# Kernel tuning notes

Measured on AMD Instinct MI355X. Metric: run time of the kernel, lower is better.

## Reference

```python
import jax, jax.numpy as jnp
import numpy as np

DECAY = 0.1  # P['decay']


def setup_inputs() -> dict:
    key = jax.random.key(0)
    k0, k1, k2, k3, k4 = jax.random.split(key, 5)
    N, B, T = 512, 64, 1024
    hidden_0 = jax.random.normal(k0, (N,), dtype=jnp.float32)
    Batch_Input = jax.random.normal(k1, (B, T, N), dtype=jnp.float32)
    # scale recurrent weight ~1/sqrt(N) so the leaky-tanh dynamics stay bounded
    W = jax.random.normal(k2, (N, N), dtype=jnp.float32) / np.sqrt(N).astype(np.float32)
    Gw = jax.random.normal(k3, (2, N), dtype=jnp.float32)
    Gb = jax.random.normal(k4, (2,), dtype=jnp.float32)
    return {"hidden_0": hidden_0, "Batch_Input": Batch_Input, "W": W, "Gw": Gw, "Gb": Gb}


def reference(hidden_0, Batch_Input, W, Gw, Gb):
    B, T, N = Batch_Input.shape
    h0 = jnp.broadcast_to(hidden_0[None, :], (B, N))  # repeat over batch
    xs = jnp.swapaxes(Batch_Input, 0, 1)  # [T, B, N] for scan over time

    def step(h, x):
        # h_new = (1-d)*h + d*(tanh(h) @ W^T + x)   (einsum 'ab,cb->ca')
        h_new = (1.0 - DECAY) * h + DECAY * (jnp.tanh(h) @ W.T + x)
        return h_new, jnp.tanh(h_new)

    _, hidden_t = jax.lax.scan(step, h0, xs)  # hidden_t: [T, B, N]
    geometry = hidden_t @ Gw.T + Gb  # [T, B, 2]
    return jnp.swapaxes(hidden_t, 0, 1), jnp.swapaxes(geometry, 0, 1)
```

## Files before the change

### kernel.cpp

```cpp
#include <hip/hip_runtime.h>
#include <hip/hip_fp16.h>
#include <cmath>

#define RN 512
#define RT 1024
#define RB 64
#define SMEM_BYTES 86016

typedef _Float16 half2v __attribute__((ext_vector_type(2)));

__device__ __forceinline__ float fast_tanh(float x) {
    float e = __expf(2.0f * x);
    return 1.0f - 2.0f / (e + 1.0f);
}
__device__ __forceinline__ unsigned pack2(float a, float b) {
    return (unsigned)__half_as_ushort(__float2half(a)) |
           ((unsigned)__half_as_ushort(__float2half(b)) << 16);
}
__device__ __forceinline__ unsigned pkrtz(float a, float b) {
    auto h = __builtin_amdgcn_cvt_pkrtz(a, b);
    return __builtin_bit_cast(unsigned, h);
}
__device__ __forceinline__ float dot2(unsigned wa, unsigned tb, float acc) {
    half2v a = __builtin_bit_cast(half2v, wa);
    half2v b = __builtin_bit_cast(half2v, tb);
    return __builtin_amdgcn_fdot2(a, b, acc, false);
}
template <int CTRL>
__device__ __forceinline__ float dpp_add(float x) {
    int p = __builtin_amdgcn_update_dpp(0, __float_as_int(x), CTRL, 0xf, 0xf, true);
    return x + __int_as_float(p);
}
__device__ __forceinline__ float red16(float x) {
    x = dpp_add<0xB1>(x);
    x = dpp_add<0x4E>(x);
    x = dpp_add<0x141>(x);
    x = dpp_add<0x140>(x);
    return x;
}
#define D2Q(acc, wq, tq) \
    acc = dot2((wq).x, (tq).x, acc); acc = dot2((wq).y, (tq).y, acc); \
    acc = dot2((wq).z, (tq).z, acc); acc = dot2((wq).w, (tq).w, acc);

#define PIN4(v) asm volatile("" : "+v"((v).x), "+v"((v).y), "+v"((v).z), "+v"((v).w));

#define LOADB(bb) { \
    const int b_ = (part + (bb)) & 3; \
    w##bb##_0 = wsrc[(b_ * 4 + 0) * 512]; PIN4(w##bb##_0) \
    w##bb##_1 = wsrc[(b_ * 4 + 1) * 512]; PIN4(w##bb##_1) \
    w##bb##_2 = wsrc[(b_ * 4 + 2) * 512]; PIN4(w##bb##_2) \
    w##bb##_3 = wsrc[(b_ * 4 + 3) * 512]; PIN4(w##bb##_3) }

#define DOTB(bb, tv) \
    D2Q(acc0, w##bb##_0, tv) D2Q(acc1, w##bb##_1, tv) \
    D2Q(acc2, w##bb##_2, tv) D2Q(acc3, w##bb##_3, tv)

__global__ void __launch_bounds__(512, 1) rnn_step_kernel(
    const float* __restrict__ h0,
    const float* __restrict__ X,
    const uint4* __restrict__ Wpk,
    const float* __restrict__ tanh0,
    float* __restrict__ outH,
    unsigned* __restrict__ ctr,
    unsigned* __restrict__ xcdctr)
{
    extern __shared__ unsigned char smem[];
    unsigned* ownpk = (unsigned*)smem;
    int*      bc    = (int*)(smem + 256);
    unsigned* lctr  = (unsigned*)(smem + 264);

    const int tid = threadIdx.x;
    if (tid == 0) {
        unsigned xcd;
        asm volatile("s_getreg_b32 %0, hwreg(HW_REG_XCC_ID)" : "=s"(xcd));
        xcd &= 7u;
        unsigned rank = __hip_atomic_fetch_add(&xcdctr[xcd], 1u,
                            __ATOMIC_RELAXED, __HIP_MEMORY_SCOPE_AGENT) & 31u;
        int slot = (int)(xcd * 32u + rank);
        bc[0] = slot >> 2;
        bc[1] = slot & 3;
        *lctr = 0u;
    }
    __syncthreads();
    const int batch = bc[0], part = bc[1];

    uint4 w0_0, w0_1, w0_2, w0_3;
    uint4 w1_0, w1_1, w1_2, w1_3;
    uint4 w2_0, w2_1, w2_2, w2_3;
    uint4 w3_0, w3_1, w3_2, w3_3;
    {
        const uint4* wsrc = Wpk + part * 8192 + tid;
        LOADB(0) LOADB(1) LOADB(2) LOADB(3)
    }

    const int rg = tid >> 4;
    const int kc = tid & 15;
    const int row0 = part * 128 + rg * 4;

    const float* srcB  = tanh0;
    const float* xPtr  = X    + (size_t)batch * RT * RN + row0;
    float*       oPtr  = outH + (size_t)batch * RT * RN + row0;
    const float* oBase = outH + (size_t)batch * RT * RN;

    float4 h = {0, 0, 0, 0};
    float4 xv = {0, 0, 0, 0};
    if (kc == 0) {
        h = *reinterpret_cast<const float4*>(h0 + row0);
        float t0 = tanhf(h.x), t1 = tanhf(h.y), t2 = tanhf(h.z), t3 = tanhf(h.w);
        ownpk[2 * rg]     = pack2(t0, t1);
        ownpk[2 * rg + 1] = pack2(t2, t3);
        xv = *reinterpret_cast<const float4*>(xPtr);
    }

    unsigned* gctr = ctr + batch * 32;
    __syncthreads();

    #pragma unroll 1
    for (int t = 0; t < RT; ++t) {
        float4 xn = {0, 0, 0, 0};
        if (kc == 0) {
            const float* xnp = (t + 1 < RT) ? (xPtr + RN) : xPtr;
            xn = *reinterpret_cast<const float4*>(xnp);
        }

        float acc0 = 0.f, acc1 = 0.f, acc2 = 0.f, acc3 = 0.f;
        {
            uint4 th = *reinterpret_cast<const uint4*>(&ownpk[4 * kc]);
            DOTB(0, th)
        }

        if (tid == 0 && t > 0) {
            const unsigned tgt = 4u * (unsigned)t;
            while (__hip_atomic_load(gctr, __ATOMIC_RELAXED,
                                     __HIP_MEMORY_SCOPE_AGENT) < tgt)
                __builtin_amdgcn_s_sleep(1);
        }
        __syncthreads();

        {
            const int b1 = (part + 1) & 3;
            const float* p = srcB + b1 * 128 + kc * 8;
            float4 f0 = *reinterpret_cast<const float4*>(p);
            float4 f1 = *reinterpret_cast<const float4*>(p + 4);
            uint4 tv = make_uint4(pkrtz(f0.x, f0.y), pkrtz(f0.z, f0.w),
                                  pkrtz(f1.x, f1.y), pkrtz(f1.z, f1.w));
            DOTB(1, tv)
        }
        {
            const int b2 = (part + 2) & 3;
            const float* p = srcB + b2 * 128 + kc * 8;
            float4 f0 = *reinterpret_cast<const float4*>(p);
            float4 f1 = *reinterpret_cast<const float4*>(p + 4);
            uint4 tv = make_uint4(pkrtz(f0.x, f0.y), pkrtz(f0.z, f0.w),
                                  pkrtz(f1.x, f1.y), pkrtz(f1.z, f1.w));
            DOTB(2, tv)
        }
        {
            const int b3 = (part + 3) & 3;
            const float* p = srcB + b3 * 128 + kc * 8;
            float4 f0 = *reinterpret_cast<const float4*>(p);
            float4 f1 = *reinterpret_cast<const float4*>(p + 4);
            uint4 tv = make_uint4(pkrtz(f0.x, f0.y), pkrtz(f0.z, f0.w),
                                  pkrtz(f1.x, f1.y), pkrtz(f1.z, f1.w));
            DOTB(3, tv)
        }

        acc0 = red16(acc0); acc1 = red16(acc1);
        acc2 = red16(acc2); acc3 = red16(acc3);

        if (kc == 0) {
            h.x = 0.9f * h.x + 0.1f * (acc0 + xv.x);
            h.y = 0.9f * h.y + 0.1f * (acc1 + xv.y);
            h.z = 0.9f * h.z + 0.1f * (acc2 + xv.z);
            h.w = 0.9f * h.w + 0.1f * (acc3 + xv.w);
            float t0 = fast_tanh(h.x), t1 = fast_tanh(h.y);
            float t2 = fast_tanh(h.z), t3 = fast_tanh(h.w);
            *reinterpret_cast<float4*>(oPtr) = make_float4(t0, t1, t2, t3);
            ownpk[2 * rg]     = pack2(t0, t1);
            ownpk[2 * rg + 1] = pack2(t2, t3);
        }

        asm volatile("s_waitcnt vmcnt(0)" ::: "memory");
        if ((tid & 63) == 0) {
            unsigned a = __hip_atomic_fetch_add(lctr, 1u, __ATOMIC_RELAXED,
                                                __HIP_MEMORY_SCOPE_WORKGROUP);
            if ((a & 7u) == 7u)
                __hip_atomic_fetch_add(gctr, 1u, __ATOMIC_RELAXED,
                                       __HIP_MEMORY_SCOPE_AGENT);
        }
        __syncthreads();
        xv = xn;

        srcB = (t == 0) ? oBase : (srcB + RN);
        xPtr += RN;
        oPtr += RN;
    }
}

__global__ void pack_w(const float* __restrict__ W, uint4* __restrict__ Wpk)
{
    int o = blockIdx.x * blockDim.x + threadIdx.x;
    if (o >= 32768) return;
    int part = o >> 13;
    int b    = (o >> 11) & 3;
    int i    = (o >> 9) & 3;
    int tid  = o & 511;
    int row  = part * 128 + (tid >> 4) * 4 + i;
    int k0   = b * 128 + (tid & 15) * 8;
    const float* s = W + (size_t)row * RN + k0;
    uint4 v;
    v.x = pack2(s[0], s[1]); v.y = pack2(s[2], s[3]);
    v.z = pack2(s[4], s[5]); v.w = pack2(s[6], s[7]);
    Wpk[o] = v;
}

__global__ void geom_kernel(const float* __restrict__ hid,
                            const float* __restrict__ Gw,
                            const float* __restrict__ Gb,
                            float* __restrict__ geo)
{
    const int wid  = (blockIdx.x * blockDim.x + threadIdx.x) >> 6;
    const int lane = threadIdx.x & 63;
    if (wid >= RB * RT) return;
    const float* rowp = hid + (size_t)wid * RN;
    float g0 = 0.f, g1 = 0.f;
    #pragma unroll
    for (int j = 0; j < 8; ++j) {
        float v = rowp[lane + 64 * j];
        g0 = fmaf(v, Gw[lane + 64 * j], g0);
        g1 = fmaf(v, Gw[RN + lane + 64 * j], g1);
    }
    #pragma unroll
    for (int m = 32; m >= 1; m >>= 1) {
        g0 += __shfl_xor(g0, m);
        g1 += __shfl_xor(g1, m);
    }
    if (lane == 0) {
        geo[(size_t)wid * 2]     = g0 + Gb[0];
        geo[(size_t)wid * 2 + 1] = g1 + Gb[1];
    }
}

__global__ void init_misc(const float* __restrict__ h0,
                          float* __restrict__ tanh0,
                          unsigned* __restrict__ ctr,
                          unsigned* __restrict__ xcdctr)
{
    int i = blockIdx.x * blockDim.x + threadIdx.x;
    if (i < RN) tanh0[i] = tanhf(h0[i]);
    if (i < RB * 32) ctr[i] = 0u;
    if (i < 8) xcdctr[i] = 0u;
}

extern "C" void kernel_launch(void* const* d_in, const int* in_sizes, int n_in,
                              void* d_out, int out_size, void* d_ws, size_t ws_size,
                              hipStream_t stream)
{
    const float* h0 = (const float*)d_in[0];
    const float* X  = (const float*)d_in[1];
    const float* W  = (const float*)d_in[2];
    const float* Gw = (const float*)d_in[3];
    const float* Gb = (const float*)d_in[4];

    float* outH = (float*)d_out;
    float* geo  = outH + (size_t)RB * RT * RN;

    float*    tanh0  = (float*)d_ws;
    unsigned* ctr    = (unsigned*)d_ws + RN;
    unsigned* xcdctr = ctr + RB * 32;
    uint4*    Wpk    = (uint4*)(((uintptr_t)(xcdctr + 8) + 63) & ~(uintptr_t)63);

    (void)hipFuncSetAttribute((const void*)rnn_step_kernel,
                              hipFuncAttributeMaxDynamicSharedMemorySize, SMEM_BYTES);

    pack_w<<<64, 512, 0, stream>>>(W, Wpk);
    init_misc<<<8, 512, 0, stream>>>(h0, tanh0, ctr, xcdctr);

    void* kargs[] = { (void*)&h0, (void*)&X, (void*)&Wpk, (void*)&tanh0,
                      (void*)&outH, (void*)&ctr, (void*)&xcdctr };
    (void)hipLaunchCooperativeKernel(rnn_step_kernel, dim3(256), dim3(512),
                                     kargs, SMEM_BYTES, stream);

    geom_kernel<<<(RB * RT * 64 + 255) / 256, 256, 0, stream>>>(outH, Gw, Gb, geo);
}
```

Baseline: 1.859 ms.

## Split each batch's recurrence across two workgroups instead of four

Each batch sequence is now handled by 2 workgroups of 256 rows each, rather than 4 workgroups of 128 rows. Each thread keeps twice as many packed fp16 weights in registers and computes 8 output rows. The upper half of the launched blocks exit immediately, and the cross-workgroup spin barrier now waits for 2 arrivals per step with no sleep. This halves the per-step cross-block synchronisation and global reads of peers' tanh outputs, but doubles per-step compute and register pressure per workgroup and leaves only 128 active CUs.

```diff
diff --git a/kernel.cpp b/kernel.cpp
--- a/kernel.cpp
+++ b/kernel.cpp
@@ -44,16 +44,20 @@
 
 #define PIN4(v) asm volatile("" : "+v"((v).x), "+v"((v).y), "+v"((v).z), "+v"((v).w));
 
-#define LOADB(bb) { \
-    const int b_ = (part + (bb)) & 3; \
-    w##bb##_0 = wsrc[(b_ * 4 + 0) * 512]; PIN4(w##bb##_0) \
-    w##bb##_1 = wsrc[(b_ * 4 + 1) * 512]; PIN4(w##bb##_1) \
-    w##bb##_2 = wsrc[(b_ * 4 + 2) * 512]; PIN4(w##bb##_2) \
-    w##bb##_3 = wsrc[(b_ * 4 + 3) * 512]; PIN4(w##bb##_3) }
-
-#define DOTB(bb, tv) \
-    D2Q(acc0, w##bb##_0, tv) D2Q(acc1, w##bb##_1, tv) \
-    D2Q(acc2, w##bb##_2, tv) D2Q(acc3, w##bb##_3, tv)
+#define DECLW(pre) uint4 pre##0_0, pre##0_1, pre##1_0, pre##1_1, pre##2_0, pre##2_1, \
+    pre##3_0, pre##3_1, pre##4_0, pre##4_1, pre##5_0, pre##5_1, pre##6_0, pre##6_1, \
+    pre##7_0, pre##7_1;
+
+#define LW(pre, base, r) \
+    pre##r##_0 = (base)[((r)*2 + 0) * 512]; PIN4(pre##r##_0) \
+    pre##r##_1 = (base)[((r)*2 + 1) * 512]; PIN4(pre##r##_1)
+
+#define LOADALL(pre, base) \
+    LW(pre, base, 0) LW(pre, base, 1) LW(pre, base, 2) LW(pre, base, 3) \
+    LW(pre, base, 4) LW(pre, base, 5) LW(pre, base, 6) LW(pre, base, 7)
+
+#define DOTA(r) D2Q(a##r, wa##r##_0, th0) D2Q(a##r, wa##r##_1, th1)
+#define DOTBq(r) D2Q(a##r, wb##r##_0, tb0) D2Q(a##r, wb##r##_1, tb1)
 
 __global__ void __launch_bounds__(512, 1) rnn_step_kernel(
     const float* __restrict__ h0,
@@ -66,8 +70,8 @@
 {
     extern __shared__ unsigned char smem[];
     unsigned* ownpk = (unsigned*)smem;
-    int*      bc    = (int*)(smem + 256);
-    unsigned* lctr  = (unsigned*)(smem + 264);
+    int*      bc    = (int*)(smem + 512);
+    unsigned* lctr  = (unsigned*)(smem + 528);
 
     const int tid = threadIdx.x;
     if (tid == 0) {
@@ -76,40 +80,49 @@
         xcd &= 7u;
         unsigned rank = __hip_atomic_fetch_add(&xcdctr[xcd], 1u,
                             __ATOMIC_RELAXED, __HIP_MEMORY_SCOPE_AGENT) & 31u;
-        int slot = (int)(xcd * 32u + rank);
-        bc[0] = slot >> 2;
-        bc[1] = slot & 3;
+        if (rank < 16u) {
+            int slot = (int)(xcd * 16u + rank);
+            bc[0] = slot >> 1;
+            bc[1] = slot & 1;
+            bc[2] = 1;
+        } else {
+            bc[2] = 0;
+        }
         *lctr = 0u;
     }
     __syncthreads();
+    if (bc[2] == 0) return;
     const int batch = bc[0], part = bc[1];
-
-    uint4 w0_0, w0_1, w0_2, w0_3;
-    uint4 w1_0, w1_1, w1_2, w1_3;
-    uint4 w2_0, w2_1, w2_2, w2_3;
-    uint4 w3_0, w3_1, w3_2, w3_3;
+    const int hfp = 1 - part;
+
+    DECLW(wa) DECLW(wb)
     {
-        const uint4* wsrc = Wpk + part * 8192 + tid;
-        LOADB(0) LOADB(1) LOADB(2) LOADB(3)
+        const uint4* wsA = Wpk + part * 16384 + part * 8192 + tid;
+        const uint4* wsB = Wpk + part * 16384 + hfp  * 8192 + tid;
+        LOADALL(wa, wsA)
+        LOADALL(wb, wsB)
     }
 
     const int rg = tid >> 4;
     const int kc = tid & 15;
-    const int row0 = part * 128 + rg * 4;
+    const int row0 = part * 256 + rg * 8;
 
     const float* srcB  = tanh0;
     const float* xPtr  = X    + (size_t)batch * RT * RN + row0;
     float*       oPtr  = outH + (size_t)batch * RT * RN + row0;
     const float* oBase = outH + (size_t)batch * RT * RN;
 
-    float4 h = {0, 0, 0, 0};
-    float4 xv = {0, 0, 0, 0};
+    float4 hA = {0,0,0,0}, hB = {0,0,0,0};
+    float4 xvA = {0,0,0,0}, xvB = {0,0,0,0};
     if (kc == 0) {
-        h = *reinterpret_cast<const float4*>(h0 + row0);
-        float t0 = tanhf(h.x), t1 = tanhf(h.y), t2 = tanhf(h.z), t3 = tanhf(h.w);
-        ownpk[2 * rg]     = pack2(t0, t1);
-        ownpk[2 * rg + 1] = pack2(t2, t3);
-        xv = *reinterpret_cast<const float4*>(xPtr);
+        hA = *reinterpret_cast<const float4*>(h0 + row0);
+        hB = *reinterpret_cast<const float4*>(h0 + row0 + 4);
+        float t0 = tanhf(hA.x), t1 = tanhf(hA.y), t2 = tanhf(hA.z), t3 = tanhf(hA.w);
+        float t4 = tanhf(hB.x), t5 = tanhf(hB.y), t6 = tanhf(hB.z), t7 = tanhf(hB.w);
+        *reinterpret_cast<uint4*>(&ownpk[rg * 4]) =
+            make_uint4(pack2(t0, t1), pack2(t2, t3), pack2(t4, t5), pack2(t6, t7));
+        xvA = *reinterpret_cast<const float4*>(xPtr);
+        xvB = *reinterpret_cast<const float4*>(xPtr + 4);
     }
 
     unsigned* gctr = ctr + batch * 32;
@@ -117,67 +130,61 @@
 
     #pragma unroll 1
     for (int t = 0; t < RT; ++t) {
-        float4 xn = {0, 0, 0, 0};
+        float4 xnA = {0,0,0,0}, xnB = {0,0,0,0};
         if (kc == 0) {
             const float* xnp = (t + 1 < RT) ? (xPtr + RN) : xPtr;
-            xn = *reinterpret_cast<const float4*>(xnp);
-        }
-
-        float acc0 = 0.f, acc1 = 0.f, acc2 = 0.f, acc3 = 0.f;
+            xnA = *reinterpret_cast<const float4*>(xnp);
+            xnB = *reinterpret_cast<const float4*>(xnp + 4);
+        }
+
+        float a0 = 0.f, a1 = 0.f, a2 = 0.f, a3 = 0.f;
+        float a4 = 0.f, a5 = 0.f, a6 = 0.f, a7 = 0.f;
         {
-            uint4 th = *reinterpret_cast<const uint4*>(&ownpk[4 * kc]);
-            DOTB(0, th)
+            uint4 th0 = *reinterpret_cast<const uint4*>(&ownpk[kc * 8]);
+            uint4 th1 = *reinterpret_cast<const uint4*>(&ownpk[kc * 8 + 4]);
+            DOTA(0) DOTA(1) DOTA(2) DOTA(3) DOTA(4) DOTA(5) DOTA(6) DOTA(7)
         }
 
         if (tid == 0 && t > 0) {
-            const unsigned tgt = 4u * (unsigned)t;
+            const unsigned tgt = 2u * (unsigned)t;
             while (__hip_atomic_load(gctr, __ATOMIC_RELAXED,
-                                     __HIP_MEMORY_SCOPE_AGENT) < tgt)
-                __builtin_amdgcn_s_sleep(1);
+                                     __HIP_MEMORY_SCOPE_AGENT) < tgt) { }
         }
         __syncthreads();
 
         {
-            const int b1 = (part + 1) & 3;
-            const float* p = srcB + b1 * 128 + kc * 8;
+            const float* p = srcB + hfp * 256 + kc * 16;
             float4 f0 = *reinterpret_cast<const float4*>(p);
             float4 f1 = *reinterpret_cast<const float4*>(p + 4);
-            uint4 tv = make_uint4(pkrtz(f0.x, f0.y), pkrtz(f0.z, f0.w),
-                                  pkrtz(f1.x, f1.y), pkrtz(f1.z, f1.w));
-            DOTB(1, tv)
-        }
-        {
-            const int b2 = (part + 2) & 3;
-            const float* p = srcB + b2 * 128 + kc * 8;
-            float4 f0 = *reinterpret_cast<const float4*>(p);
-            float4 f1 = *reinterpret_cast<const float4*>(p + 4);
-            uint4 tv = make_uint4(pkrtz(f0.x, f0.y), pkrtz(f0.z, f0.w),
-                                  pkrtz(f1.x, f1.y), pkrtz(f1.z, f1.w));
-            DOTB(2, tv)
-        }
-        {
-            const int b3 = (part + 3) & 3;
-            const float* p = srcB + b3 * 128 + kc * 8;
-            float4 f0 = *reinterpret_cast<const float4*>(p);
-            float4 f1 = *reinterpret_cast<const float4*>(p + 4);
-            uint4 tv = make_uint4(pkrtz(f0.x, f0.y), pkrtz(f0.z, f0.w),
-                                  pkrtz(f1.x, f1.y), pkrtz(f1.z, f1.w));
-            DOTB(3, tv)
-        }
-
-        acc0 = red16(acc0); acc1 = red16(acc1);
-        acc2 = red16(acc2); acc3 = red16(acc3);
+            float4 f2 = *reinterpret_cast<const float4*>(p + 8);
+            float4 f3 = *reinterpret_cast<const float4*>(p + 12);
+            uint4 tb0 = make_uint4(pkrtz(f0.x, f0.y), pkrtz(f0.z, f0.w),
+                                   pkrtz(f1.x, f1.y), pkrtz(f1.z, f1.w));
+            uint4 tb1 = make_uint4(pkrtz(f2.x, f2.y), pkrtz(f2.z, f2.w),
+                                   pkrtz(f3.x, f3.y), pkrtz(f3.z, f3.w));
+            DOTBq(0) DOTBq(1) DOTBq(2) DOTBq(3) DOTBq(4) DOTBq(5) DOTBq(6) DOTBq(7)
+        }
+
+        a0 = red16(a0); a1 = red16(a1); a2 = red16(a2); a3 = red16(a3);
+        a4 = red16(a4); a5 = red16(a5); a6 = red16(a6); a7 = red16(a7);
 
         if (kc == 0) {
-            h.x = 0.9f * h.x + 0.1f * (acc0 + xv.x);
-            h.y = 0.9f * h.y + 0.1f * (acc1 + xv.y);
-            h.z = 0.9f * h.z + 0.1f * (acc2 + xv.z);
-            h.w = 0.9f * h.w + 0.1f * (acc3 + xv.w);
-            float t0 = fast_tanh(h.x), t1 = fast_tanh(h.y);
-            float t2 = fast_tanh(h.z), t3 = fast_tanh(h.w);
-            *reinterpret_cast<float4*>(oPtr) = make_float4(t0, t1, t2, t3);
-            ownpk[2 * rg]     = pack2(t0, t1);
-            ownpk[2 * rg + 1] = pack2(t2, t3);
+            hA.x = 0.9f * hA.x + 0.1f * (a0 + xvA.x);
+            hA.y = 0.9f * hA.y + 0.1f * (a1 + xvA.y);
+            hA.z = 0.9f * hA.z + 0.1f * (a2 + xvA.z);
+            hA.w = 0.9f * hA.w + 0.1f * (a3 + xvA.w);
+            hB.x = 0.9f * hB.x + 0.1f * (a4 + xvB.x);
+            hB.y = 0.9f * hB.y + 0.1f * (a5 + xvB.y);
+            hB.z = 0.9f * hB.z + 0.1f * (a6 + xvB.z);
+            hB.w = 0.9f * hB.w + 0.1f * (a7 + xvB.w);
+            float t0 = fast_tanh(hA.x), t1 = fast_tanh(hA.y);
+            float t2 = fast_tanh(hA.z), t3 = fast_tanh(hA.w);
+            float t4 = fast_tanh(hB.x), t5 = fast_tanh(hB.y);
+            float t6 = fast_tanh(hB.z), t7 = fast_tanh(hB.w);
+            *reinterpret_cast<float4*>(oPtr)     = make_float4(t0, t1, t2, t3);
+            *reinterpret_cast<float4*>(oPtr + 4) = make_float4(t4, t5, t6, t7);
+            *reinterpret_cast<uint4*>(&ownpk[rg * 4]) =
+                make_uint4(pack2(t0, t1), pack2(t2, t3), pack2(t4, t5), pack2(t6, t7));
         }
 
         asm volatile("s_waitcnt vmcnt(0)" ::: "memory");
@@ -189,7 +196,7 @@
                                        __HIP_MEMORY_SCOPE_AGENT);
         }
         __syncthreads();
-        xv = xn;
+        xvA = xnA; xvB = xnB;
 
         srcB = (t == 0) ? oBase : (srcB + RN);
         xPtr += RN;
@@ -201,13 +208,14 @@
 {
     int o = blockIdx.x * blockDim.x + threadIdx.x;
     if (o >= 32768) return;
-    int part = o >> 13;
-    int b    = (o >> 11) & 3;
-    int i    = (o >> 9) & 3;
-    int tid  = o & 511;
-    int row  = part * 128 + (tid >> 4) * 4 + i;
-    int k0   = b * 128 + (tid & 15) * 8;
-    const float* s = W + (size_t)row * RN + k0;
+    int p   = o >> 14;
+    int hf  = (o >> 13) & 1;
+    int k   = (o >> 9) & 15;
+    int tid = o & 511;
+    int r = k >> 1, j = k & 1;
+    int row = p * 256 + (tid >> 4) * 8 + r;
+    int col = hf * 256 + (tid & 15) * 16 + j * 8;
+    const float* s = W + (size_t)row * RN + col;
     uint4 v;
     v.x = pack2(s[0], s[1]); v.y = pack2(s[2], s[3]);
     v.z = pack2(s[4], s[5]); v.w = pack2(s[6], s[7]);
```

Result: slower. 2.435 ms (+31.0%).
